# Optimization experiments

Hardware: AMD Instinct MI355X
Metric: run time of the kernel (lower is better)

## Reference

```python
import jax, jax.numpy as jnp
import numpy as np

N = 50000        # nodes
E = 800000       # edges (before self-loops)
F_IN = 128       # input features
HID = 32         # per-head hidden channels
H1 = 4           # heads of conv1
H2 = 8           # heads of conv2
NEG_SLOPE = 0.2  # PyG GATConv LeakyReLU slope
E_DEC = 100000   # pos/neg decode edges each


def setup_inputs() -> dict:
    key = jax.random.key(0)
    ks = jax.random.split(key, 12)
    s = 0.1
    return {
        "x": jax.random.normal(ks[0], (N, F_IN), jnp.float32),
        "edge_index": jax.random.randint(ks[1], (2, E), 0, N, dtype=jnp.int32),
        "pos_edge_index": jax.random.randint(ks[2], (2, E_DEC), 0, N, dtype=jnp.int32),
        "neg_edge_index": jax.random.randint(ks[3], (2, E_DEC), 0, N, dtype=jnp.int32),
        "W1": jax.random.normal(ks[4], (F_IN, H1 * HID), jnp.float32) * s,
        "a_src1": jax.random.normal(ks[5], (H1, HID), jnp.float32) * s,
        "a_dst1": jax.random.normal(ks[6], (H1, HID), jnp.float32) * s,
        "b1": jax.random.normal(ks[7], (H1 * HID,), jnp.float32) * s,
        "W2": jax.random.normal(ks[8], (H1 * HID, H2 * HID), jnp.float32) * s,
        "a_src2": jax.random.normal(ks[9], (H2, HID), jnp.float32) * s,
        "a_dst2": jax.random.normal(ks[10], (H2, HID), jnp.float32) * s,
        "b2": jax.random.normal(ks[11], (H2 * HID,), jnp.float32) * s,
    }


def _segment_softmax(e, seg, n):
    # softmax over edges grouped by destination node; max is detached (cancels analytically)
    m = jax.lax.stop_gradient(jax.ops.segment_max(e, seg, num_segments=n))
    ex = jnp.exp(e - m[seg])
    denom = jax.ops.segment_sum(ex, seg, num_segments=n)
    return ex / (denom[seg] + 1e-16)


def _gat_conv(x, src, dst, W, a_src, a_dst, b, heads, out_ch):
    n = x.shape[0]
    h = (x @ W).reshape(n, heads, out_ch)             # [N,H,C]
    al_s = (h * a_src[None]).sum(-1)                  # [N,H]
    al_d = (h * a_dst[None]).sum(-1)                  # [N,H]
    e = al_s[src] + al_d[dst]                         # [E,H] edge logits
    e = jnp.where(e > 0, e, NEG_SLOPE * e)            # LeakyReLU
    alpha = _segment_softmax(e, dst, n)               # [E,H]
    msg = h[src] * alpha[:, :, None]                  # [E,H,C]
    out = jax.ops.segment_sum(msg, dst, num_segments=n)  # [N,H,C]
    return out.reshape(n, heads * out_ch) + b


def reference(x, edge_index, pos_edge_index, neg_edge_index,
              W1, a_src1, a_dst1, b1, W2, a_src2, a_dst2, b2):
    n = x.shape[0]
    loops = jnp.arange(n, dtype=edge_index.dtype)     # PyG add_self_loops=True
    src = jnp.concatenate([edge_index[0], loops])
    dst = jnp.concatenate([edge_index[1], loops])
    # encode
    z = jax.nn.relu(_gat_conv(x, src, dst, W1, a_src1, a_dst1, b1, H1, HID))
    z = _gat_conv(z, src, dst, W2, a_src2, a_dst2, b2, H2, HID)
    # decode
    ei = jnp.concatenate([pos_edge_index, neg_edge_index], axis=1)
    logits = (z[ei[0]] * z[ei[1]]).sum(-1)            # [2*E_DEC]
    return logits
```

## Files before the change

### kernel.cpp

```cpp
#include <hip/hip_runtime.h>
#include <hip/hip_bf16.h>

#define NN 50000
#define EE 800000
#define ET (EE + NN)
#define F_IN 128
#define HID 32
#define H1 4
#define H2 8
#define E_DEC 100000
#define NEG_SLOPE 0.2f

typedef __attribute__((ext_vector_type(8))) short short8;
typedef __attribute__((ext_vector_type(4))) float floatx4;

__device__ __forceinline__ unsigned short f2b(float f) {
    __hip_bfloat16 h = __float2bfloat16(f);
    return *reinterpret_cast<unsigned short*>(&h);
}
__device__ __forceinline__ float b2f(unsigned short u) {
    return __uint_as_float(((unsigned int)u) << 16);
}

__device__ __forceinline__ void packW_one(const float* __restrict__ W,
                                          unsigned short* __restrict__ Wp, int OUT, int id) {
    const int ctg = id >> 8;
    const int ln = id & 63;
    const int col = ctg * 16 + (ln & 15);
    const int k0 = ((id >> 6) & 3) * 32 + ((ln >> 4) & 3) * 8;
    ushort4 lo, hi;
    lo.x = f2b(W[(k0 + 0) * OUT + col]);
    lo.y = f2b(W[(k0 + 1) * OUT + col]);
    lo.z = f2b(W[(k0 + 2) * OUT + col]);
    lo.w = f2b(W[(k0 + 3) * OUT + col]);
    hi.x = f2b(W[(k0 + 4) * OUT + col]);
    hi.y = f2b(W[(k0 + 5) * OUT + col]);
    hi.z = f2b(W[(k0 + 6) * OUT + col]);
    hi.w = f2b(W[(k0 + 7) * OUT + col]);
    ((ushort4*)Wp)[id * 2] = lo;
    ((ushort4*)Wp)[id * 2 + 1] = hi;
}

#define HIST_BLOCKS ((EE / 4 + 255) / 256)
#define PACK_BLOCKS ((6144 + 255) / 256)

__global__ void hist_pack_k(const int* __restrict__ ei, int* __restrict__ counts_p,
                            const int* __restrict__ probe, int* __restrict__ rank,
                            const float* __restrict__ W1, unsigned short* __restrict__ wp1,
                            const float* __restrict__ W2, unsigned short* __restrict__ wp2) {
    if (blockIdx.x < HIST_BLOCKS) {
        const int t = blockIdx.x * 256 + threadIdx.x;
        if (t >= EE / 4) return;
        const int pv = probe[0];
        int* cp = counts_p + (blockIdx.x & 7) * NN;
        const int4 d4 = ((const int4*)(ei + EE))[t];
        int4 r4;
        r4.x = atomicAdd(&cp[d4.x], 1) - pv;
        r4.y = atomicAdd(&cp[d4.y], 1) - pv;
        r4.z = atomicAdd(&cp[d4.z], 1) - pv;
        r4.w = atomicAdd(&cp[d4.w], 1) - pv;
        ((int4*)rank)[t] = r4;
    } else {
        const int id = (blockIdx.x - HIST_BLOCKS) * 256 + threadIdx.x;
        if (id < 2048) packW_one(W1, wp1, 128, id);
        else if (id < 6144) packW_one(W2, wp2, 256, id - 2048);
    }
}

__global__ void scan1_k(const int* __restrict__ counts_p, const int* __restrict__ probe,
                        int* __restrict__ bsum) {
    __shared__ int sh[256];
    const unsigned pv = (unsigned)probe[0];
    int t = threadIdx.x;
    int i = blockIdx.x * 256 + t;
    int deg = 0;
    if (i < NN) {
        unsigned sum = 0;
#pragma unroll
        for (int s = 0; s < 8; ++s) sum += (unsigned)counts_p[s * NN + i];
        deg = (int)(sum - 8u * pv) + 1;
    }
    sh[t] = deg;
    __syncthreads();
    for (int off = 128; off > 0; off >>= 1) {
        if (t < off) sh[t] += sh[t + off];
        __syncthreads();
    }
    if (t == 0) bsum[blockIdx.x] = sh[0];
}

__global__ void scan2_k(int* __restrict__ bsum, int nb, int* __restrict__ start) {
    __shared__ int sh[256];
    int t = threadIdx.x;
    int v = (t < nb) ? bsum[t] : 0;
    sh[t] = v;
    __syncthreads();
    for (int off = 1; off < 256; off <<= 1) {
        int u = (t >= off) ? sh[t - off] : 0;
        __syncthreads();
        sh[t] += u;
        __syncthreads();
    }
    if (t < nb) bsum[t] = sh[t] - v;
    if (t == 0) start[NN] = ET;
}

__global__ void scan3_k(const int* __restrict__ counts_p, const int* __restrict__ probe,
                        const int* __restrict__ bsum, int* __restrict__ start,
                        int* __restrict__ offs, int* __restrict__ csr) {
    __shared__ int sh[256];
    const unsigned pv = (unsigned)probe[0];
    int t = threadIdx.x;
    int i = blockIdx.x * 256 + t;
    int part[8];
    int deg = 0;
    if (i < NN) {
        deg = 1;
#pragma unroll
        for (int s = 0; s < 8; ++s) {
            part[s] = (int)((unsigned)counts_p[s * NN + i] - pv);
            deg += part[s];
        }
    }
    sh[t] = deg;
    __syncthreads();
    for (int off = 1; off < 256; off <<= 1) {
        int u = (t >= off) ? sh[t - off] : 0;
        __syncthreads();
        sh[t] += u;
        __syncthreads();
    }
    int excl = sh[t] - deg + bsum[blockIdx.x];
    if (i < NN) {
        start[i] = excl;
        int o = excl;
#pragma unroll
        for (int s = 0; s < 8; ++s) {
            offs[s * NN + i] = o;
            o += part[s];
        }
        csr[o] = i;
    }
}

__global__ void scatter_k(const int* __restrict__ ei, const int* __restrict__ rank,
                          const int* __restrict__ offs, int* __restrict__ csr) {
    const int t = blockIdx.x * 256 + threadIdx.x;
    if (t >= EE / 4) return;
    const int* off = offs + (blockIdx.x & 7) * NN;
    const int4 s4 = ((const int4*)ei)[t];
    const int4 d4 = ((const int4*)(ei + EE))[t];
    const int4 r4 = ((const int4*)rank)[t];
    csr[off[d4.x] + r4.x] = s4.x;
    csr[off[d4.y] + r4.y] = s4.y;
    csr[off[d4.z] + r4.z] = s4.z;
    csr[off[d4.w] + r4.w] = s4.w;
}

template <int OUT, int H, int CT, bool F32IN>
__global__ void gemm_k(const void* __restrict__ Xin, const unsigned short* __restrict__ Wp,
                       const float* __restrict__ a_src, const float* __restrict__ a_dst,
                       unsigned short* __restrict__ Hout, float* __restrict__ als,
                       float* __restrict__ ald) {
    const int wave = threadIdx.x >> 6;
    const int lane = threadIdx.x & 63;
    const int quad = lane >> 4;
    const int rl = lane & 15;
    const int r0 = blockIdx.x * 64;
    floatx4 acc[4][CT];
#pragma unroll
    for (int rt = 0; rt < 4; ++rt)
#pragma unroll
        for (int ct = 0; ct < CT; ++ct) acc[rt][ct] = {0.f, 0.f, 0.f, 0.f};

#pragma unroll
    for (int ks = 0; ks < 4; ++ks) {
        short8 a[4];
        const int c0k = ks * 32 + quad * 8;
#pragma unroll
        for (int rt = 0; rt < 4; ++rt) {
            int row = r0 + rt * 16 + rl;
            row = row < NN ? row : NN - 1;
            if (F32IN) {
                const float4* xp =
                    (const float4*)((const float*)Xin + (long long)row * 128 + c0k);
                const float4 v0 = xp[0];
                const float4 v1 = xp[1];
                short8 tt;
                tt[0] = (short)f2b(v0.x);
                tt[1] = (short)f2b(v0.y);
                tt[2] = (short)f2b(v0.z);
                tt[3] = (short)f2b(v0.w);
                tt[4] = (short)f2b(v1.x);
                tt[5] = (short)f2b(v1.y);
                tt[6] = (short)f2b(v1.z);
                tt[7] = (short)f2b(v1.w);
                a[rt] = tt;
            } else {
                a[rt] = *(const short8*)((const unsigned short*)Xin +
                                         (long long)row * 128 + c0k);
            }
        }
#pragma unroll
        for (int ct = 0; ct < CT; ++ct) {
            const int ctg = wave * CT + ct;
            const short8 b = *(const short8*)(Wp + (((ctg * 4 + ks) * 64 + lane) << 3));
#pragma unroll
            for (int rt = 0; rt < 4; ++rt)
                acc[rt][ct] = __builtin_amdgcn_mfma_f32_16x16x32_bf16(a[rt], b, acc[rt][ct], 0, 0, 0);
        }
    }
#pragma unroll
    for (int rt = 0; rt < 4; ++rt) {
        const int rowbase = r0 + rt * 16 + quad * 4;
#pragma unroll
        for (int ct = 0; ct < CT; ++ct) {
            const int col = (wave * CT + ct) * 16 + rl;
#pragma unroll
            for (int r = 0; r < 4; ++r) {
                const int row = rowbase + r;
                if (row < NN) Hout[(long long)row * OUT + col] = f2b(acc[rt][ct][r]);
            }
        }
    }
    float asv[CT], adv[CT];
#pragma unroll
    for (int ct = 0; ct < CT; ++ct) {
        const int col = (wave * CT + ct) * 16 + rl;
        asv[ct] = a_src[col];
        adv[ct] = a_dst[col];
    }
#pragma unroll
    for (int rt = 0; rt < 4; ++rt) {
#pragma unroll
        for (int r = 0; r < 4; ++r) {
            const int row = r0 + rt * 16 + quad * 4 + r;
            float ps[CT / 2], pd[CT / 2];
#pragma unroll
            for (int hh = 0; hh < CT / 2; ++hh) {
                ps[hh] = acc[rt][2 * hh][r] * asv[2 * hh] + acc[rt][2 * hh + 1][r] * asv[2 * hh + 1];
                pd[hh] = acc[rt][2 * hh][r] * adv[2 * hh] + acc[rt][2 * hh + 1][r] * adv[2 * hh + 1];
#pragma unroll
                for (int m = 8; m >= 1; m >>= 1) {
                    ps[hh] += __shfl_xor(ps[hh], m, 64);
                    pd[hh] += __shfl_xor(pd[hh], m, 64);
                }
            }
            if (rl == 0 && row < NN) {
#pragma unroll
                for (int hh = 0; hh < CT / 2; ++hh) {
                    const int hd = wave * (CT / 2) + hh;
                    als[(long long)row * H + hd] = ps[hh];
                    ald[(long long)row * H + hd] = pd[hh];
                }
            }
        }
    }
}

__global__ void gather1_k(const int* __restrict__ start, const int* __restrict__ csr,
                          const float* __restrict__ als, const float* __restrict__ ald,
                          const unsigned short* __restrict__ Hin,
                          const float* __restrict__ bias, unsigned short* __restrict__ outp) {
    const int d = blockIdx.x;
    const int lane = threadIdx.x;
    const int cl = lane & 31;
    const int slot = lane >> 5;
    const int hd = cl >> 3;
    const int beg = start[d], end = start[d + 1];
    const float aldd = ald[(long long)d * H1 + hd];
    float a0 = 0.f, a1 = 0.f, a2 = 0.f, a3 = 0.f, den = 0.f;
    int i = beg + slot;
    for (; i + 7 * 2 < end; i += 8 * 2) {
        int s[8];
        float l[8];
        ushort4 hv[8];
#pragma unroll
        for (int k = 0; k < 8; ++k) s[k] = csr[i + k * 2];
#pragma unroll
        for (int k = 0; k < 8; ++k) l[k] = als[(long long)s[k] * H1 + hd] + aldd;
#pragma unroll
        for (int k = 0; k < 8; ++k) hv[k] = *(const ushort4*)(Hin + (long long)s[k] * 128 + cl * 4);
#pragma unroll
        for (int k = 0; k < 8; ++k) {
            float lg = l[k] > 0.f ? l[k] : NEG_SLOPE * l[k];
            const float w = __expf(lg);
            den += w;
            a0 += w * b2f(hv[k].x);
            a1 += w * b2f(hv[k].y);
            a2 += w * b2f(hv[k].z);
            a3 += w * b2f(hv[k].w);
        }
    }
    for (; i + 3 * 2 < end; i += 4 * 2) {
        int s[4];
        float l[4];
        ushort4 hv[4];
#pragma unroll
        for (int k = 0; k < 4; ++k) s[k] = csr[i + k * 2];
#pragma unroll
        for (int k = 0; k < 4; ++k) l[k] = als[(long long)s[k] * H1 + hd] + aldd;
#pragma unroll
        for (int k = 0; k < 4; ++k) hv[k] = *(const ushort4*)(Hin + (long long)s[k] * 128 + cl * 4);
#pragma unroll
        for (int k = 0; k < 4; ++k) {
            float lg = l[k] > 0.f ? l[k] : NEG_SLOPE * l[k];
            const float w = __expf(lg);
            den += w;
            a0 += w * b2f(hv[k].x);
            a1 += w * b2f(hv[k].y);
            a2 += w * b2f(hv[k].z);
            a3 += w * b2f(hv[k].w);
        }
    }
    for (; i < end; i += 2) {
        const int s = csr[i];
        float lg = als[(long long)s * H1 + hd] + aldd;
        lg = lg > 0.f ? lg : NEG_SLOPE * lg;
        const float w = __expf(lg);
        const ushort4 hv = *(const ushort4*)(Hin + (long long)s * 128 + cl * 4);
        den += w;
        a0 += w * b2f(hv.x);
        a1 += w * b2f(hv.y);
        a2 += w * b2f(hv.z);
        a3 += w * b2f(hv.w);
    }
    a0 += __shfl_xor(a0, 32, 64);
    a1 += __shfl_xor(a1, 32, 64);
    a2 += __shfl_xor(a2, 32, 64);
    a3 += __shfl_xor(a3, 32, 64);
    den += __shfl_xor(den, 32, 64);
    if (lane < 32) {
        const float inv = 1.f / (den + 1e-16f);
        const int c0 = cl * 4;
        float v0 = a0 * inv + bias[c0];
        float v1 = a1 * inv + bias[c0 + 1];
        float v2 = a2 * inv + bias[c0 + 2];
        float v3 = a3 * inv + bias[c0 + 3];
        v0 = v0 > 0.f ? v0 : 0.f;
        v1 = v1 > 0.f ? v1 : 0.f;
        v2 = v2 > 0.f ? v2 : 0.f;
        v3 = v3 > 0.f ? v3 : 0.f;
        ushort4 o;
        o.x = f2b(v0);
        o.y = f2b(v1);
        o.z = f2b(v2);
        o.w = f2b(v3);
        *(ushort4*)(outp + (long long)d * 128 + c0) = o;
    }
}

__global__ void gather2_k(const int* __restrict__ start, const int* __restrict__ csr,
                          const float* __restrict__ als, const float* __restrict__ ald,
                          const unsigned short* __restrict__ Hin,
                          const float* __restrict__ bias, unsigned short* __restrict__ outp) {
    const int d = blockIdx.x;
    const int lane = threadIdx.x;
    const int hd = lane >> 3;
    const int beg = start[d], end = start[d + 1];
    const float aldd = ald[(long long)d * H2 + hd];
    float a0 = 0.f, a1 = 0.f, a2 = 0.f, a3 = 0.f, den = 0.f;
    int i = beg;
    for (; i + 7 < end; i += 8) {
        int s[8];
        float l[8];
        ushort4 hv[8];
#pragma unroll
        for (int k = 0; k < 8; ++k) s[k] = csr[i + k];
#pragma unroll
        for (int k = 0; k < 8; ++k) l[k] = als[(long long)s[k] * H2 + hd] + aldd;
#pragma unroll
        for (int k = 0; k < 8; ++k) hv[k] = *(const ushort4*)(Hin + (long long)s[k] * 256 + lane * 4);
#pragma unroll
        for (int k = 0; k < 8; ++k) {
            float lg = l[k] > 0.f ? l[k] : NEG_SLOPE * l[k];
            const float w = __expf(lg);
            den += w;
            a0 += w * b2f(hv[k].x);
            a1 += w * b2f(hv[k].y);
            a2 += w * b2f(hv[k].z);
            a3 += w * b2f(hv[k].w);
        }
    }
    for (; i + 3 < end; i += 4) {
        int s[4];
        float l[4];
        ushort4 hv[4];
#pragma unroll
        for (int k = 0; k < 4; ++k) s[k] = csr[i + k];
#pragma unroll
        for (int k = 0; k < 4; ++k) l[k] = als[(long long)s[k] * H2 + hd] + aldd;
#pragma unroll
        for (int k = 0; k < 4; ++k) hv[k] = *(const ushort4*)(Hin + (long long)s[k] * 256 + lane * 4);
#pragma unroll
        for (int k = 0; k < 4; ++k) {
            float lg = l[k] > 0.f ? l[k] : NEG_SLOPE * l[k];
            const float w = __expf(lg);
            den += w;
            a0 += w * b2f(hv[k].x);
            a1 += w * b2f(hv[k].y);
            a2 += w * b2f(hv[k].z);
            a3 += w * b2f(hv[k].w);
        }
    }
    for (; i < end; ++i) {
        const int s = csr[i];
        float lg = als[(long long)s * H2 + hd] + aldd;
        lg = lg > 0.f ? lg : NEG_SLOPE * lg;
        const float w = __expf(lg);
        const ushort4 hv = *(const ushort4*)(Hin + (long long)s * 256 + lane * 4);
        den += w;
        a0 += w * b2f(hv.x);
        a1 += w * b2f(hv.y);
        a2 += w * b2f(hv.z);
        a3 += w * b2f(hv.w);
    }
    const float inv = 1.f / (den + 1e-16f);
    const int c0 = lane * 4;
    ushort4 o;
    o.x = f2b(a0 * inv + bias[c0]);
    o.y = f2b(a1 * inv + bias[c0 + 1]);
    o.z = f2b(a2 * inv + bias[c0 + 2]);
    o.w = f2b(a3 * inv + bias[c0 + 3]);
    *(ushort4*)(outp + (long long)d * 256 + c0) = o;
}

__global__ void decode_s_k(const int* __restrict__ pei, const int* __restrict__ nei,
                           const unsigned short* __restrict__ z2, float* __restrict__ part) {
    const int s = blockIdx.x & 7;
    const int g = blockIdx.x >> 3;
    const int wave = threadIdx.x >> 6, lane = threadIdx.x & 63;
    const int slot = lane >> 3, cl = lane & 7;
    const int idx = g * 32 + wave * 8 + slot;
    if (idx >= 2 * E_DEC) return;
    int a, b;
    if (idx < E_DEC) {
        a = pei[idx];
        b = pei[E_DEC + idx];
    } else {
        const int j = idx - E_DEC;
        a = nei[j];
        b = nei[E_DEC + j];
    }
    const ushort4 ua = *(const ushort4*)(z2 + (long long)a * 256 + s * 32 + cl * 4);
    const ushort4 ub = *(const ushort4*)(z2 + (long long)b * 256 + s * 32 + cl * 4);
    float sum = b2f(ua.x) * b2f(ub.x) + b2f(ua.y) * b2f(ub.y) +
                b2f(ua.z) * b2f(ub.z) + b2f(ua.w) * b2f(ub.w);
    sum += __shfl_xor(sum, 4, 64);
    sum += __shfl_xor(sum, 2, 64);
    sum += __shfl_xor(sum, 1, 64);
    if (cl == 0) part[(long long)s * (2 * E_DEC) + idx] = sum;
}

__global__ void reduce_k(const float* __restrict__ part, float* __restrict__ out) {
    const int i = blockIdx.x * 256 + threadIdx.x;
    if (i >= 2 * E_DEC) return;
    float s = 0.f;
#pragma unroll
    for (int k = 0; k < 8; ++k) s += part[(long long)k * (2 * E_DEC) + i];
    out[i] = s;
}

extern "C" void kernel_launch(void* const* d_in, const int* in_sizes, int n_in,
                              void* d_out, int out_size, void* d_ws, size_t ws_size,
                              hipStream_t stream) {
    const float* x = (const float*)d_in[0];
    const int* ei = (const int*)d_in[1];
    const int* pei = (const int*)d_in[2];
    const int* nei = (const int*)d_in[3];
    const float* W1 = (const float*)d_in[4];
    const float* as1 = (const float*)d_in[5];
    const float* ad1 = (const float*)d_in[6];
    const float* b1 = (const float*)d_in[7];
    const float* W2 = (const float*)d_in[8];
    const float* as2 = (const float*)d_in[9];
    const float* ad2 = (const float*)d_in[10];
    const float* b2 = (const float*)d_in[11];
    float* out = (float*)d_out;

    unsigned short* h1 = (unsigned short*)d_ws;
    unsigned short* h2 = h1 + (long long)NN * 128;
    unsigned short* z2 = h2 + (long long)NN * 256;
    unsigned short* z1 = z2 + (long long)NN * 256;
    unsigned short* wp1 = z1 + (long long)NN * 128;
    unsigned short* wp2 = wp1 + 128 * 128;
    float* als1 = (float*)(wp2 + 128 * 256);
    float* ald1 = als1 + NN * H1;
    float* als2 = ald1 + NN * H1;
    float* ald2 = als2 + NN * H2;
    float* part = ald2 + NN * H2;
    int* counts_p = (int*)(part + 8 * 2 * E_DEC);
    int* start = counts_p + 8 * NN;
    int* offs = start + NN + 1;
    int* rank = offs + 8 * NN;
    int* bsum = rank + EE;
    int* csr = bsum + 256;
    int* probe = csr + ET;

    const int NB = (NN + 255) / 256;

    hist_pack_k<<<HIST_BLOCKS + PACK_BLOCKS, 256, 0, stream>>>(
        ei, counts_p, probe, rank, W1, wp1, W2, wp2);
    scan1_k<<<NB, 256, 0, stream>>>(counts_p, probe, bsum);
    scan2_k<<<1, 256, 0, stream>>>(bsum, NB, start);
    scan3_k<<<NB, 256, 0, stream>>>(counts_p, probe, bsum, start, offs, csr);
    scatter_k<<<HIST_BLOCKS, 256, 0, stream>>>(ei, rank, offs, csr);

    gemm_k<128, H1, 2, true><<<(NN + 63) / 64, 256, 0, stream>>>(
        x, wp1, as1, ad1, h1, als1, ald1);
    gather1_k<<<NN, 64, 0, stream>>>(start, csr, als1, ald1, h1, b1, z1);

    gemm_k<256, H2, 4, false><<<(NN + 63) / 64, 256, 0, stream>>>(
        z1, wp2, as2, ad2, h2, als2, ald2);
    gather2_k<<<NN, 64, 0, stream>>>(start, csr, als2, ald2, h2, b2, z2);

    decode_s_k<<<8 * ((2 * E_DEC + 31) / 32), 256, 0, stream>>>(pei, nei, z2, part);
    reduce_k<<<(2 * E_DEC + 255) / 256, 256, 0, stream>>>(part, out);
}
```

Baseline: 334.7 us.

## Head-major layout and degree-sorted multi-node gather for second GAT layer

The second-layer GEMM now writes features and attention logits in head-major slabs, so each head's 32 channels for all nodes are contiguous. The new gather kernel processes one head per block slice, with 8 lanes per destination node and 32 nodes per block. Nodes are visited in degree-sorted order via a counting sort built from a degree histogram, so each wave gets similar trip counts. The aim is better cache locality for the per-head gathers and less load imbalance than one 64-thread block per node. The cost is two extra small kernels, an atomic histogram, and strided output writes to z2.

```diff
diff --git a/kernel.cpp b/kernel.cpp
--- a/kernel.cpp
+++ b/kernel.cpp
@@ -89,9 +89,11 @@
     if (t == 0) bsum[blockIdx.x] = sh[0];
 }
 
-__global__ void scan2_k(int* __restrict__ bsum, int nb, int* __restrict__ start) {
+__global__ void scan2_k(int* __restrict__ bsum, int nb, int* __restrict__ start,
+                        int* __restrict__ dbin) {
     __shared__ int sh[256];
     int t = threadIdx.x;
+    dbin[t] = 0;
     int v = (t < nb) ? bsum[t] : 0;
     sh[t] = v;
     __syncthreads();
@@ -107,8 +109,10 @@
 
 __global__ void scan3_k(const int* __restrict__ counts_p, const int* __restrict__ probe,
                         const int* __restrict__ bsum, int* __restrict__ start,
-                        int* __restrict__ offs, int* __restrict__ csr) {
+                        int* __restrict__ offs, int* __restrict__ csr,
+                        int* __restrict__ dbin) {
     __shared__ int sh[256];
+    __shared__ int lh[256];
     const unsigned pv = (unsigned)probe[0];
     int t = threadIdx.x;
     int i = blockIdx.x * 256 + t;
@@ -122,6 +126,7 @@
             deg += part[s];
         }
     }
+    lh[t] = 0;
     sh[t] = deg;
     __syncthreads();
     for (int off = 1; off < 256; off <<= 1) {
@@ -140,7 +145,46 @@
             o += part[s];
         }
         csr[o] = i;
-    }
+        atomicAdd(&lh[deg > 255 ? 255 : deg], 1);
+    }
+    __syncthreads();
+    if (lh[t] > 0) atomicAdd(&dbin[t], lh[t]);
+}
+
+__global__ void dscan_k(const int* __restrict__ dbin, int* __restrict__ dcur) {
+    __shared__ int sh[256];
+    int t = threadIdx.x;
+    int v = dbin[t];
+    sh[t] = v;
+    __syncthreads();
+    for (int off = 1; off < 256; off <<= 1) {
+        int u = (t >= off) ? sh[t - off] : 0;
+        __syncthreads();
+        sh[t] += u;
+        __syncthreads();
+    }
+    dcur[t] = sh[t] - v;
+}
+
+__global__ void dsort_k(const int* __restrict__ start, int* __restrict__ dcur,
+                        int* __restrict__ perm) {
+    __shared__ int lh[256];
+    __shared__ int lbase[256];
+    const int t = threadIdx.x;
+    const int i = blockIdx.x * 256 + t;
+    lh[t] = 0;
+    __syncthreads();
+    int deg = 0, lr = 0;
+    if (i < NN) {
+        deg = start[i + 1] - start[i];
+        if (deg > 255) deg = 255;
+        lr = atomicAdd(&lh[deg], 1);
+    }
+    __syncthreads();
+    const int cnt = lh[t];
+    if (cnt > 0) lbase[t] = atomicAdd(&dcur[t], cnt);
+    __syncthreads();
+    if (i < NN) perm[lbase[deg] + lr] = i;
 }
 
 __global__ void scatter_k(const int* __restrict__ ei, const int* __restrict__ rank,
@@ -157,7 +201,7 @@
     csr[off[d4.w] + r4.w] = s4.w;
 }
 
-template <int OUT, int H, int CT, bool F32IN>
+template <int OUT, int H, int CT, bool F32IN, int HSCH, bool ALS_HM>
 __global__ void gemm_k(const void* __restrict__ Xin, const unsigned short* __restrict__ Wp,
                        const float* __restrict__ a_src, const float* __restrict__ a_dst,
                        unsigned short* __restrict__ Hout, float* __restrict__ als,
@@ -216,10 +260,11 @@
 #pragma unroll
         for (int ct = 0; ct < CT; ++ct) {
             const int col = (wave * CT + ct) * 16 + rl;
+            const long long sb = (long long)(col / HSCH) * NN * HSCH + (col % HSCH);
 #pragma unroll
             for (int r = 0; r < 4; ++r) {
                 const int row = rowbase + r;
-                if (row < NN) Hout[(long long)row * OUT + col] = f2b(acc[rt][ct][r]);
+                if (row < NN) Hout[sb + (long long)row * HSCH] = f2b(acc[rt][ct][r]);
             }
         }
     }
@@ -250,8 +295,10 @@
 #pragma unroll
                 for (int hh = 0; hh < CT / 2; ++hh) {
                     const int hd = wave * (CT / 2) + hh;
-                    als[(long long)row * H + hd] = ps[hh];
-                    ald[(long long)row * H + hd] = pd[hh];
+                    const long long ai = ALS_HM ? ((long long)hd * NN + row)
+                                                : ((long long)row * H + hd);
+                    als[ai] = ps[hh];
+                    ald[ai] = pd[hh];
                 }
             }
         }
@@ -350,27 +397,36 @@
     }
 }
 
-__global__ void gather2_k(const int* __restrict__ start, const int* __restrict__ csr,
-                          const float* __restrict__ als, const float* __restrict__ ald,
-                          const unsigned short* __restrict__ Hin,
-                          const float* __restrict__ bias, unsigned short* __restrict__ outp) {
-    const int d = blockIdx.x;
-    const int lane = threadIdx.x;
-    const int hd = lane >> 3;
+__global__ void gather2s_k(const int* __restrict__ start, const int* __restrict__ csr,
+                           const int* __restrict__ perm,
+                           const float* __restrict__ als, const float* __restrict__ ald,
+                           const unsigned short* __restrict__ h2s,
+                           const float* __restrict__ bias, unsigned short* __restrict__ z2) {
+    const int s = blockIdx.x & 7;
+    const int g = blockIdx.x >> 3;
+    const int wave = threadIdx.x >> 6;
+    const int lane = threadIdx.x & 63;
+    const int slot = lane >> 3;
+    const int cl = lane & 7;
+    const int idx = g * 32 + wave * 8 + slot;
+    if (idx >= NN) return;
+    const int d = perm[idx];
+    const float* alsh = als + (long long)s * NN;
+    const unsigned short* hsl = h2s + (long long)s * NN * 32 + cl * 4;
     const int beg = start[d], end = start[d + 1];
-    const float aldd = ald[(long long)d * H2 + hd];
+    const float aldd = ald[(long long)s * NN + d];
     float a0 = 0.f, a1 = 0.f, a2 = 0.f, a3 = 0.f, den = 0.f;
     int i = beg;
     for (; i + 7 < end; i += 8) {
-        int s[8];
+        int sx[8];
         float l[8];
         ushort4 hv[8];
 #pragma unroll
-        for (int k = 0; k < 8; ++k) s[k] = csr[i + k];
-#pragma unroll
-        for (int k = 0; k < 8; ++k) l[k] = als[(long long)s[k] * H2 + hd] + aldd;
-#pragma unroll
-        for (int k = 0; k < 8; ++k) hv[k] = *(const ushort4*)(Hin + (long long)s[k] * 256 + lane * 4);
+        for (int k = 0; k < 8; ++k) sx[k] = csr[i + k];
+#pragma unroll
+        for (int k = 0; k < 8; ++k) l[k] = alsh[sx[k]] + aldd;
+#pragma unroll
+        for (int k = 0; k < 8; ++k) hv[k] = *(const ushort4*)(hsl + (long long)sx[k] * 32);
 #pragma unroll
         for (int k = 0; k < 8; ++k) {
             float lg = l[k] > 0.f ? l[k] : NEG_SLOPE * l[k];
@@ -383,15 +439,15 @@
         }
     }
     for (; i + 3 < end; i += 4) {
-        int s[4];
+        int sx[4];
         float l[4];
         ushort4 hv[4];
 #pragma unroll
-        for (int k = 0; k < 4; ++k) s[k] = csr[i + k];
-#pragma unroll
-        for (int k = 0; k < 4; ++k) l[k] = als[(long long)s[k] * H2 + hd] + aldd;
-#pragma unroll
-        for (int k = 0; k < 4; ++k) hv[k] = *(const ushort4*)(Hin + (long long)s[k] * 256 + lane * 4);
+        for (int k = 0; k < 4; ++k) sx[k] = csr[i + k];
+#pragma unroll
+        for (int k = 0; k < 4; ++k) l[k] = alsh[sx[k]] + aldd;
+#pragma unroll
+        for (int k = 0; k < 4; ++k) hv[k] = *(const ushort4*)(hsl + (long long)sx[k] * 32);
 #pragma unroll
         for (int k = 0; k < 4; ++k) {
             float lg = l[k] > 0.f ? l[k] : NEG_SLOPE * l[k];
@@ -404,11 +460,11 @@
         }
     }
     for (; i < end; ++i) {
-        const int s = csr[i];
-        float lg = als[(long long)s * H2 + hd] + aldd;
+        const int sx = csr[i];
+        float lg = alsh[sx] + aldd;
         lg = lg > 0.f ? lg : NEG_SLOPE * lg;
         const float w = __expf(lg);
-        const ushort4 hv = *(const ushort4*)(Hin + (long long)s * 256 + lane * 4);
+        const ushort4 hv = *(const ushort4*)(hsl + (long long)sx * 32);
         den += w;
         a0 += w * b2f(hv.x);
         a1 += w * b2f(hv.y);
@@ -416,13 +472,13 @@
         a3 += w * b2f(hv.w);
     }
     const float inv = 1.f / (den + 1e-16f);
-    const int c0 = lane * 4;
+    const float4 bv = *(const float4*)(bias + s * 32 + cl * 4);
     ushort4 o;
-    o.x = f2b(a0 * inv + bias[c0]);
-    o.y = f2b(a1 * inv + bias[c0 + 1]);
-    o.z = f2b(a2 * inv + bias[c0 + 2]);
-    o.w = f2b(a3 * inv + bias[c0 + 3]);
-    *(ushort4*)(outp + (long long)d * 256 + c0) = o;
+    o.x = f2b(a0 * inv + bv.x);
+    o.y = f2b(a1 * inv + bv.y);
+    o.z = f2b(a2 * inv + bv.z);
+    o.w = f2b(a3 * inv + bv.w);
+    *(ushort4*)(z2 + (long long)d * 256 + s * 32 + cl * 4) = o;
 }
 
 __global__ void decode_s_k(const int* __restrict__ pei, const int* __restrict__ nei,
@@ -479,8 +535,8 @@
     float* out = (float*)d_out;
 
     unsigned short* h1 = (unsigned short*)d_ws;
-    unsigned short* h2 = h1 + (long long)NN * 128;
-    unsigned short* z2 = h2 + (long long)NN * 256;
+    unsigned short* h2s = h1 + (long long)NN * 128;
+    unsigned short* z2 = h2s + (long long)NN * 256;
     unsigned short* z1 = z2 + (long long)NN * 256;
     unsigned short* wp1 = z1 + (long long)NN * 128;
     unsigned short* wp2 = wp1 + 128 * 128;
@@ -494,7 +550,10 @@
     int* offs = start + NN + 1;
     int* rank = offs + 8 * NN;
     int* bsum = rank + EE;
-    int* csr = bsum + 256;
+    int* dbin = bsum + 256;
+    int* dcur = dbin + 256;
+    int* perm = dcur + 256;
+    int* csr = perm + NN;
     int* probe = csr + ET;
 
     const int NB = (NN + 255) / 256;
@@ -502,17 +561,20 @@
     hist_pack_k<<<HIST_BLOCKS + PACK_BLOCKS, 256, 0, stream>>>(
         ei, counts_p, probe, rank, W1, wp1, W2, wp2);
     scan1_k<<<NB, 256, 0, stream>>>(counts_p, probe, bsum);
-    scan2_k<<<1, 256, 0, stream>>>(bsum, NB, start);
-    scan3_k<<<NB, 256, 0, stream>>>(counts_p, probe, bsum, start, offs, csr);
+    scan2_k<<<1, 256, 0, stream>>>(bsum, NB, start, dbin);
+    scan3_k<<<NB, 256, 0, stream>>>(counts_p, probe, bsum, start, offs, csr, dbin);
+    dscan_k<<<1, 256, 0, stream>>>(dbin, dcur);
+    dsort_k<<<NB, 256, 0, stream>>>(start, dcur, perm);
     scatter_k<<<HIST_BLOCKS, 256, 0, stream>>>(ei, rank, offs, csr);
 
-    gemm_k<128, H1, 2, true><<<(NN + 63) / 64, 256, 0, stream>>>(
+    gemm_k<128, H1, 2, true, 128, false><<<(NN + 63) / 64, 256, 0, stream>>>(
         x, wp1, as1, ad1, h1, als1, ald1);
     gather1_k<<<NN, 64, 0, stream>>>(start, csr, als1, ald1, h1, b1, z1);
 
-    gemm_k<256, H2, 4, false><<<(NN + 63) / 64, 256, 0, stream>>>(
-        z1, wp2, as2, ad2, h2, als2, ald2);
-    gather2_k<<<NN, 64, 0, stream>>>(start, csr, als2, ald2, h2, b2, z2);
+    gemm_k<256, H2, 4, false, 32, true><<<(NN + 63) / 64, 256, 0, stream>>>(
+        z1, wp2, as2, ad2, h2s, als2, ald2);
+    gather2s_k<<<8 * ((NN + 31) / 32), 256, 0, stream>>>(
+        start, csr, perm, als2, ald2, h2s, b2, z2);
 
     decode_s_k<<<8 * ((2 * E_DEC + 31) / 32), 256, 0, stream>>>(pei, nei, z2, part);
     reduce_k<<<(2 * E_DEC + 255) / 256, 256, 0, stream>>>(part, out);
```

Measured after the change: 360.8 us. 1.08x slower.

## Fuse three-kernel prefix scan into single kernel with grid-wide spin barrier

Applied to the files above, without the earlier changes.

Replaces the scan1/scan2/scan3 kernel sequence with one kernel: each block computes its local scan, publishes its block total, then spins on a global atomic counter until all 196 blocks arrive before scanning the block totals itself. The counter is reset by an extra block in the histogram/pack kernel. This removes two kernel launches and the extra read of the count arrays, at the risk of deadlock if not all 196 blocks are co-resident and some added spin overhead.

```diff
diff --git a/kernel.cpp b/kernel.cpp
--- a/kernel.cpp
+++ b/kernel.cpp
@@ -10,6 +10,7 @@
 #define H2 8
 #define E_DEC 100000
 #define NEG_SLOPE 0.2f
+#define NB_SCAN 196
 
 typedef __attribute__((ext_vector_type(8))) short short8;
 typedef __attribute__((ext_vector_type(4))) float floatx4;
@@ -47,7 +48,8 @@
 __global__ void hist_pack_k(const int* __restrict__ ei, int* __restrict__ counts_p,
                             const int* __restrict__ probe, int* __restrict__ rank,
                             const float* __restrict__ W1, unsigned short* __restrict__ wp1,
-                            const float* __restrict__ W2, unsigned short* __restrict__ wp2) {
+                            const float* __restrict__ W2, unsigned short* __restrict__ wp2,
+                            int* __restrict__ done) {
     if (blockIdx.x < HIST_BLOCKS) {
         const int t = blockIdx.x * 256 + threadIdx.x;
         if (t >= EE / 4) return;
@@ -64,54 +66,20 @@
         const int id = (blockIdx.x - HIST_BLOCKS) * 256 + threadIdx.x;
         if (id < 2048) packW_one(W1, wp1, 128, id);
         else if (id < 6144) packW_one(W2, wp2, 256, id - 2048);
-    }
-}
-
-__global__ void scan1_k(const int* __restrict__ counts_p, const int* __restrict__ probe,
-                        int* __restrict__ bsum) {
+        else if (id == 6144) done[0] = 0;
+    }
+}
+
+__global__ void scanfused_k(const int* __restrict__ counts_p, const int* __restrict__ probe,
+                            int* __restrict__ agg, int* __restrict__ done,
+                            int* __restrict__ start, int* __restrict__ offs,
+                            int* __restrict__ csr) {
     __shared__ int sh[256];
+    __shared__ int sh2[256];
     const unsigned pv = (unsigned)probe[0];
-    int t = threadIdx.x;
-    int i = blockIdx.x * 256 + t;
-    int deg = 0;
-    if (i < NN) {
-        unsigned sum = 0;
-#pragma unroll
-        for (int s = 0; s < 8; ++s) sum += (unsigned)counts_p[s * NN + i];
-        deg = (int)(sum - 8u * pv) + 1;
-    }
-    sh[t] = deg;
-    __syncthreads();
-    for (int off = 128; off > 0; off >>= 1) {
-        if (t < off) sh[t] += sh[t + off];
-        __syncthreads();
-    }
-    if (t == 0) bsum[blockIdx.x] = sh[0];
-}
-
-__global__ void scan2_k(int* __restrict__ bsum, int nb, int* __restrict__ start) {
-    __shared__ int sh[256];
-    int t = threadIdx.x;
-    int v = (t < nb) ? bsum[t] : 0;
-    sh[t] = v;
-    __syncthreads();
-    for (int off = 1; off < 256; off <<= 1) {
-        int u = (t >= off) ? sh[t - off] : 0;
-        __syncthreads();
-        sh[t] += u;
-        __syncthreads();
-    }
-    if (t < nb) bsum[t] = sh[t] - v;
-    if (t == 0) start[NN] = ET;
-}
-
-__global__ void scan3_k(const int* __restrict__ counts_p, const int* __restrict__ probe,
-                        const int* __restrict__ bsum, int* __restrict__ start,
-                        int* __restrict__ offs, int* __restrict__ csr) {
-    __shared__ int sh[256];
-    const unsigned pv = (unsigned)probe[0];
-    int t = threadIdx.x;
-    int i = blockIdx.x * 256 + t;
+    const int t = threadIdx.x;
+    const int b = blockIdx.x;
+    const int i = b * 256 + t;
     int part[8];
     int deg = 0;
     if (i < NN) {
@@ -130,7 +98,23 @@
         sh[t] += u;
         __syncthreads();
     }
-    int excl = sh[t] - deg + bsum[blockIdx.x];
+    if (t == 0) {
+        agg[b] = sh[255];
+        __threadfence();
+        atomicAdd(&done[0], 1);
+        while (atomicAdd(&done[0], 0) < NB_SCAN) __builtin_amdgcn_s_sleep(8);
+    }
+    __syncthreads();
+    sh2[t] = (t < NB_SCAN) ? agg[t] : 0;
+    __syncthreads();
+    for (int off = 1; off < 256; off <<= 1) {
+        int u = (t >= off) ? sh2[t - off] : 0;
+        __syncthreads();
+        sh2[t] += u;
+        __syncthreads();
+    }
+    const int base = (b > 0) ? sh2[b - 1] : 0;
+    const int excl = base + sh[t] - deg;
     if (i < NN) {
         start[i] = excl;
         int o = excl;
@@ -141,6 +125,7 @@
         }
         csr[o] = i;
     }
+    if (b == 0 && t == 0) start[NN] = ET;
 }
 
 __global__ void scatter_k(const int* __restrict__ ei, const int* __restrict__ rank,
@@ -493,17 +478,14 @@
     int* start = counts_p + 8 * NN;
     int* offs = start + NN + 1;
     int* rank = offs + 8 * NN;
-    int* bsum = rank + EE;
-    int* csr = bsum + 256;
+    int* agg = rank + EE;
+    int* done = agg + 256;
+    int* csr = done + 1;
     int* probe = csr + ET;
 
-    const int NB = (NN + 255) / 256;
-
-    hist_pack_k<<<HIST_BLOCKS + PACK_BLOCKS, 256, 0, stream>>>(
-        ei, counts_p, probe, rank, W1, wp1, W2, wp2);
-    scan1_k<<<NB, 256, 0, stream>>>(counts_p, probe, bsum);
-    scan2_k<<<1, 256, 0, stream>>>(bsum, NB, start);
-    scan3_k<<<NB, 256, 0, stream>>>(counts_p, probe, bsum, start, offs, csr);
+    hist_pack_k<<<HIST_BLOCKS + PACK_BLOCKS + 1, 256, 0, stream>>>(
+        ei, counts_p, probe, rank, W1, wp1, W2, wp2, done);
+    scanfused_k<<<NB_SCAN, 256, 0, stream>>>(counts_p, probe, agg, done, start, offs, csr);
     scatter_k<<<HIST_BLOCKS, 256, 0, stream>>>(ei, rank, offs, csr);
 
     gemm_k<128, H1, 2, true><<<(NN + 63) / 64, 256, 0, stream>>>(
```

Result: no change. 339.7 us (+1.5%).
